# Optimization experiments

Hardware: AMD Instinct MI355X
Metric: run time of the kernel (lower is better)

## Reference

```python
import jax, jax.numpy as jnp
import numpy as np

EMBED = 1024
HEAD = 64
CTX = 2048


def setup_inputs() -> dict:
    key = jax.random.key(0)
    ks = jax.random.split(key, 7)
    scale = 1.0 / np.sqrt(EMBED)
    return {
        "x": jax.random.normal(ks[0], (8, CTX, EMBED), dtype=jnp.float32),
        "Wq": jax.random.normal(ks[1], (EMBED, HEAD), dtype=jnp.float32) * scale,
        "bq": jax.random.normal(ks[2], (HEAD,), dtype=jnp.float32) * 0.01,
        "Wk": jax.random.normal(ks[3], (EMBED, HEAD), dtype=jnp.float32) * scale,
        "bk": jax.random.normal(ks[4], (HEAD,), dtype=jnp.float32) * 0.01,
        "Wv": jax.random.normal(ks[5], (EMBED, HEAD), dtype=jnp.float32) * scale,
        "bv": jax.random.normal(ks[6], (HEAD,), dtype=jnp.float32) * 0.01,
    }


def reference(x, Wq, bq, Wk, bk, Wv, bv):
    # x: [B, T, E]
    q = x @ Wq + bq  # [B, T, H]
    k = x @ Wk + bk
    v = x @ Wv + bv
    scores = jnp.einsum("bqh,bkh->bqk", q, k) / jnp.sqrt(jnp.float32(HEAD))
    T = x.shape[1]
    causal = jnp.tril(jnp.ones((T, T), dtype=bool))
    scores = jnp.where(causal, scores, -jnp.inf)
    attn = jax.nn.softmax(scores, axis=-1)  # dropout=0.0 -> identity
    out = jnp.einsum("bqk,bkh->bqh", attn, v)
    return out
```

## Files before the change

kernel.cpp:

```cpp
#include <hip/hip_runtime.h>
#include <math.h>
#include <stdint.h>

#define BDIM 8
#define TDIM 2048
#define EDIM 1024
#define HDIM 64
#define NCHUNK 144

typedef short bf16x8 __attribute__((ext_vector_type(8)));
typedef float f32x4 __attribute__((ext_vector_type(4)));

__device__ __forceinline__ unsigned short f2bf(float f) {
    uint32_t u = __builtin_bit_cast(uint32_t, f);
    u += 0x7fffu + ((u >> 16) & 1u);
    return (unsigned short)(u >> 16);
}
__device__ __forceinline__ float bf2f(unsigned short s) {
    uint32_t u = ((uint32_t)s) << 16;
    return __builtin_bit_cast(float, u);
}

__global__ __launch_bounds__(256) void prep_w(
    const float* __restrict__ Wq, const float* __restrict__ Wk,
    const float* __restrict__ Wv,
    unsigned short* __restrict__ WqT, unsigned short* __restrict__ WkT,
    unsigned short* __restrict__ WvT)
{
    int id = blockIdx.x * 256 + threadIdx.x;
    int e = id >> 6, h = id & 63;
    int oi = h * EDIM + e;
    WqT[oi] = f2bf(Wq[id]);
    WkT[oi] = f2bf(Wk[id]);
    WvT[oi] = f2bf(Wv[id]);
}

__global__ __launch_bounds__(256) void proj_kernel(
    const float* __restrict__ x,
    const unsigned short* __restrict__ WqT, const unsigned short* __restrict__ WkT,
    const unsigned short* __restrict__ WvT,
    const float* __restrict__ bq, const float* __restrict__ bk,
    const float* __restrict__ bv,
    unsigned short* __restrict__ Qb, unsigned short* __restrict__ Kb,
    unsigned short* __restrict__ VbT)
{
    __shared__ unsigned short Xs[2][64][72];
    __shared__ unsigned short Wqs[2][64][72];
    __shared__ unsigned short Wks[2][64][72];
    __shared__ unsigned short Wvs[2][64][72];

    const int t = threadIdx.x;
    const int lane = t & 63, w = t >> 6, quad = lane >> 4, ln = lane & 15;
    const int row0 = blockIdx.x * 64;
    const int sr = t >> 2;
    const int sc = (t & 3) << 4;

    f32x4 accq[4], acck[4], accv[4];
#pragma unroll
    for (int j = 0; j < 4; ++j) {
        accq[j] = (f32x4)(0.f); acck[j] = (f32x4)(0.f); accv[j] = (f32x4)(0.f);
    }

    const float* xp0  = &x[(size_t)(row0 + sr) * EDIM + sc];
    const size_t wrow = (size_t)sr * EDIM + sc;

    {
        float4 x0 = *(const float4*)(xp0);
        float4 x1 = *(const float4*)(xp0 + 4);
        float4 x2 = *(const float4*)(xp0 + 8);
        float4 x3 = *(const float4*)(xp0 + 12);
        bf16x8 xb0, xb1;
        xb0[0]=(short)f2bf(x0.x); xb0[1]=(short)f2bf(x0.y); xb0[2]=(short)f2bf(x0.z); xb0[3]=(short)f2bf(x0.w);
        xb0[4]=(short)f2bf(x1.x); xb0[5]=(short)f2bf(x1.y); xb0[6]=(short)f2bf(x1.z); xb0[7]=(short)f2bf(x1.w);
        xb1[0]=(short)f2bf(x2.x); xb1[1]=(short)f2bf(x2.y); xb1[2]=(short)f2bf(x2.z); xb1[3]=(short)f2bf(x2.w);
        xb1[4]=(short)f2bf(x3.x); xb1[5]=(short)f2bf(x3.y); xb1[6]=(short)f2bf(x3.z); xb1[7]=(short)f2bf(x3.w);
        *(bf16x8*)&Xs[0][sr][sc]     = xb0;
        *(bf16x8*)&Xs[0][sr][sc + 8] = xb1;
        *(bf16x8*)&Wqs[0][sr][sc]     = *(const bf16x8*)&WqT[wrow];
        *(bf16x8*)&Wqs[0][sr][sc + 8] = *(const bf16x8*)&WqT[wrow + 8];
        *(bf16x8*)&Wks[0][sr][sc]     = *(const bf16x8*)&WkT[wrow];
        *(bf16x8*)&Wks[0][sr][sc + 8] = *(const bf16x8*)&WkT[wrow + 8];
        *(bf16x8*)&Wvs[0][sr][sc]     = *(const bf16x8*)&WvT[wrow];
        *(bf16x8*)&Wvs[0][sr][sc + 8] = *(const bf16x8*)&WvT[wrow + 8];
    }

    for (int kt = 0; kt < EDIM / 64; ++kt) {
        const int cur = kt & 1, nxt = cur ^ 1;

        float4 x0, x1, x2, x3;
        bf16x8 wq0, wq1, wk0, wk1, wv0, wv1;
        if (kt < 15) {
            const float* xp = xp0 + (kt + 1) * 64;
            x0 = *(const float4*)(xp);
            x1 = *(const float4*)(xp + 4);
            x2 = *(const float4*)(xp + 8);
            x3 = *(const float4*)(xp + 12);
            const size_t wo = wrow + (kt + 1) * 64;
            wq0 = *(const bf16x8*)&WqT[wo];
            wq1 = *(const bf16x8*)&WqT[wo + 8];
            wk0 = *(const bf16x8*)&WkT[wo];
            wk1 = *(const bf16x8*)&WkT[wo + 8];
            wv0 = *(const bf16x8*)&WvT[wo];
            wv1 = *(const bf16x8*)&WvT[wo + 8];
        }

        __syncthreads();

        bf16x8 xa0 = *(const bf16x8*)&Xs[cur][16 * w + ln][8 * quad];
        bf16x8 xa1 = *(const bf16x8*)&Xs[cur][16 * w + ln][32 + 8 * quad];
#pragma unroll
        for (int j = 0; j < 4; ++j) {
            bf16x8 w0, w1;
            w0 = *(const bf16x8*)&Wqs[cur][16 * j + ln][8 * quad];
            w1 = *(const bf16x8*)&Wqs[cur][16 * j + ln][32 + 8 * quad];
            accq[j] = __builtin_amdgcn_mfma_f32_16x16x32_bf16(xa0, w0, accq[j], 0, 0, 0);
            accq[j] = __builtin_amdgcn_mfma_f32_16x16x32_bf16(xa1, w1, accq[j], 0, 0, 0);
            w0 = *(const bf16x8*)&Wks[cur][16 * j + ln][8 * quad];
            w1 = *(const bf16x8*)&Wks[cur][16 * j + ln][32 + 8 * quad];
            acck[j] = __builtin_amdgcn_mfma_f32_16x16x32_bf16(xa0, w0, acck[j], 0, 0, 0);
            acck[j] = __builtin_amdgcn_mfma_f32_16x16x32_bf16(xa1, w1, acck[j], 0, 0, 0);
            w0 = *(const bf16x8*)&Wvs[cur][16 * j + ln][8 * quad];
            w1 = *(const bf16x8*)&Wvs[cur][16 * j + ln][32 + 8 * quad];
            accv[j] = __builtin_amdgcn_mfma_f32_16x16x32_bf16(xa0, w0, accv[j], 0, 0, 0);
            accv[j] = __builtin_amdgcn_mfma_f32_16x16x32_bf16(xa1, w1, accv[j], 0, 0, 0);
        }

        if (kt < 15) {
            bf16x8 xb0, xb1;
            xb0[0]=(short)f2bf(x0.x); xb0[1]=(short)f2bf(x0.y); xb0[2]=(short)f2bf(x0.z); xb0[3]=(short)f2bf(x0.w);
            xb0[4]=(short)f2bf(x1.x); xb0[5]=(short)f2bf(x1.y); xb0[6]=(short)f2bf(x1.z); xb0[7]=(short)f2bf(x1.w);
            xb1[0]=(short)f2bf(x2.x); xb1[1]=(short)f2bf(x2.y); xb1[2]=(short)f2bf(x2.z); xb1[3]=(short)f2bf(x2.w);
            xb1[4]=(short)f2bf(x3.x); xb1[5]=(short)f2bf(x3.y); xb1[6]=(short)f2bf(x3.z); xb1[7]=(short)f2bf(x3.w);
            *(bf16x8*)&Xs[nxt][sr][sc]     = xb0;
            *(bf16x8*)&Xs[nxt][sr][sc + 8] = xb1;
            *(bf16x8*)&Wqs[nxt][sr][sc]     = wq0;
            *(bf16x8*)&Wqs[nxt][sr][sc + 8] = wq1;
            *(bf16x8*)&Wks[nxt][sr][sc]     = wk0;
            *(bf16x8*)&Wks[nxt][sr][sc + 8] = wk1;
            *(bf16x8*)&Wvs[nxt][sr][sc]     = wv0;
            *(bf16x8*)&Wvs[nxt][sr][sc + 8] = wv1;
        }
    }

#pragma unroll
    for (int j = 0; j < 4; ++j) {
        int col = 16 * j + ln;
        float bqv = bq[col], bkv = bk[col], bvv = bv[col];
#pragma unroll
        for (int r = 0; r < 4; ++r) {
            size_t row = (size_t)(row0 + 16 * w + 4 * quad + r);
            Qb[row * HDIM + col] = f2bf(accq[j][r] + bqv);
            Kb[row * HDIM + col] = f2bf(acck[j][r] + bkv);
            int bb = (int)(row >> 11);
            int tr = (int)(row & 2047);
            VbT[((size_t)bb * HDIM + col) * TDIM + tr] = f2bf(accv[j][r] + bvv);
        }
    }
}

__global__ __launch_bounds__(256) void attn_partial(
    const unsigned short* __restrict__ Qb, const unsigned short* __restrict__ Kb,
    const unsigned short* __restrict__ VbT,
    unsigned short* __restrict__ PO, float* __restrict__ Pm, float* __restrict__ Pl)
{
    __shared__ unsigned short Ks[2][64][72];
    __shared__ unsigned short VsT[2][64][72];
    __shared__ unsigned short Ps[64][72];

    const int t = threadIdx.x;
    const int lane = t & 63, w = t >> 6, quad = lane >> 4, ln = lane & 15;
    const int f = blockIdx.x;
    const int b = blockIdx.y;

    int g = 0;
    while (f >= 2 * (g + 1) * (g + 2)) ++g;
    const int r_  = f - 2 * g * (g + 1);
    const int iq  = 4 * g + r_ / (g + 1);
    const int ch  = r_ % (g + 1);

    const int q0 = iq * 64;
    const size_t base = (size_t)b * TDIM * HDIM;
    const int sr = t >> 2;
    const int sc = (t & 3) << 4;

    const size_t qrow = base + (size_t)(q0 + 16 * w + ln) * HDIM;
    bf16x8 qa0 = *(const bf16x8*)&Qb[qrow + 8 * quad];
    bf16x8 qa1 = *(const bf16x8*)&Qb[qrow + 32 + 8 * quad];

    f32x4 od[4];
#pragma unroll
    for (int j = 0; j < 4; ++j) od[j] = (f32x4)(0.f);
    float mrow[4], lrow[4];
#pragma unroll
    for (int r = 0; r < 4; ++r) { mrow[r] = -INFINITY; lrow[r] = 0.f; }

    const float scale = 0.125f;
    const int jt0 = 4 * ch;
    int j1 = jt0 + 3; if (j1 > iq) j1 = iq;

    {
        size_t ko = base + (size_t)(jt0 * 64 + sr) * HDIM + sc;
        *(bf16x8*)&Ks[0][sr][sc]     = *(const bf16x8*)&Kb[ko];
        *(bf16x8*)&Ks[0][sr][sc + 8] = *(const bf16x8*)&Kb[ko + 8];
        const unsigned short* vrow =
            &VbT[((size_t)b * HDIM + sr) * TDIM + jt0 * 64 + sc];
        *(bf16x8*)&VsT[0][sr][sc]     = *(const bf16x8*)vrow;
        *(bf16x8*)&VsT[0][sr][sc + 8] = *(const bf16x8*)(vrow + 8);
    }

    for (int jt = jt0; jt <= j1; ++jt) {
        const int cur = (jt - jt0) & 1, nxt = cur ^ 1;

        bf16x8 kn0, kn1, vn0, vn1;
        if (jt < j1) {
            size_t ko = base + (size_t)((jt + 1) * 64 + sr) * HDIM + sc;
            kn0 = *(const bf16x8*)&Kb[ko];
            kn1 = *(const bf16x8*)&Kb[ko + 8];
            const unsigned short* vrow =
                &VbT[((size_t)b * HDIM + sr) * TDIM + (jt + 1) * 64 + sc];
            vn0 = *(const bf16x8*)vrow;
            vn1 = *(const bf16x8*)(vrow + 8);
        }

        __syncthreads();

        f32x4 s[4];
#pragma unroll
        for (int j = 0; j < 4; ++j) {
            bf16x8 kb0 = *(const bf16x8*)&Ks[cur][16 * j + ln][8 * quad];
            bf16x8 kb1 = *(const bf16x8*)&Ks[cur][16 * j + ln][32 + 8 * quad];
            s[j] = (f32x4)(0.f);
            s[j] = __builtin_amdgcn_mfma_f32_16x16x32_bf16(qa0, kb0, s[j], 0, 0, 0);
            s[j] = __builtin_amdgcn_mfma_f32_16x16x32_bf16(qa1, kb1, s[j], 0, 0, 0);
        }

        if (jt == iq) {
#pragma unroll
            for (int j = 0; j < 4; ++j) {
                int kg = jt * 64 + 16 * j + ln;
#pragma unroll
                for (int r = 0; r < 4; ++r) {
                    int qg = q0 + 16 * w + 4 * quad + r;
                    s[j][r] = (kg <= qg) ? s[j][r] * scale : -INFINITY;
                }
            }
        } else {
#pragma unroll
            for (int j = 0; j < 4; ++j)
#pragma unroll
                for (int r = 0; r < 4; ++r) s[j][r] *= scale;
        }

        float mx[4];
#pragma unroll
        for (int r = 0; r < 4; ++r)
            mx[r] = fmaxf(fmaxf(s[0][r], s[1][r]), fmaxf(s[2][r], s[3][r]));
#pragma unroll
        for (int d = 1; d < 16; d <<= 1)
#pragma unroll
            for (int r = 0; r < 4; ++r)
                mx[r] = fmaxf(mx[r], __shfl_xor(mx[r], d));

        float al[4], rs[4];
#pragma unroll
        for (int r = 0; r < 4; ++r) {
            float mn = fmaxf(mrow[r], mx[r]);
            al[r] = __expf(mrow[r] - mn);
            mrow[r] = mn;
            float p0 = __expf(s[0][r] - mn);
            float p1 = __expf(s[1][r] - mn);
            float p2 = __expf(s[2][r] - mn);
            float p3 = __expf(s[3][r] - mn);
            s[0][r] = p0; s[1][r] = p1; s[2][r] = p2; s[3][r] = p3;
            rs[r] = (p0 + p1) + (p2 + p3);
        }
#pragma unroll
        for (int d = 1; d < 16; d <<= 1)
#pragma unroll
            for (int r = 0; r < 4; ++r)
                rs[r] += __shfl_xor(rs[r], d);
#pragma unroll
        for (int r = 0; r < 4; ++r) lrow[r] = lrow[r] * al[r] + rs[r];

#pragma unroll
        for (int j = 0; j < 4; ++j)
#pragma unroll
            for (int r = 0; r < 4; ++r) {
                od[j][r] *= al[r];
                Ps[16 * w + 4 * quad + r][16 * j + ln] = f2bf(s[j][r]);
            }

        bf16x8 pa0 = *(const bf16x8*)&Ps[16 * w + ln][8 * quad];
        bf16x8 pa1 = *(const bf16x8*)&Ps[16 * w + ln][32 + 8 * quad];
#pragma unroll
        for (int j = 0; j < 4; ++j) {
            bf16x8 vb0 = *(const bf16x8*)&VsT[cur][16 * j + ln][8 * quad];
            bf16x8 vb1 = *(const bf16x8*)&VsT[cur][16 * j + ln][32 + 8 * quad];
            od[j] = __builtin_amdgcn_mfma_f32_16x16x32_bf16(pa0, vb0, od[j], 0, 0, 0);
            od[j] = __builtin_amdgcn_mfma_f32_16x16x32_bf16(pa1, vb1, od[j], 0, 0, 0);
        }

        if (jt < j1) {
            *(bf16x8*)&Ks[nxt][sr][sc]     = kn0;
            *(bf16x8*)&Ks[nxt][sr][sc + 8] = kn1;
            *(bf16x8*)&VsT[nxt][sr][sc]     = vn0;
            *(bf16x8*)&VsT[nxt][sr][sc + 8] = vn1;
        }
    }

    const size_t p = (size_t)b * NCHUNK + f;
#pragma unroll
    for (int j = 0; j < 4; ++j)
#pragma unroll
        for (int r = 0; r < 4; ++r)
            PO[p * 4096 + (size_t)(16 * w + 4 * quad + r) * 64 + 16 * j + ln] =
                f2bf(od[j][r]);
    if (ln == 0) {
#pragma unroll
        for (int r = 0; r < 4; ++r) {
            Pm[p * 64 + 16 * w + 4 * quad + r] = mrow[r];
            Pl[p * 64 + 16 * w + 4 * quad + r] = lrow[r];
        }
    }
}

__global__ __launch_bounds__(256) void attn_combine(
    const unsigned short* __restrict__ PO, const float* __restrict__ Pm,
    const float* __restrict__ Pl, float* __restrict__ out)
{
    const int iq = blockIdx.x, b = blockIdx.y;
    const int g = iq >> 2;
    const int nch = g + 1;
    const int fbase = 2 * g * (g + 1) + (iq - 4 * g) * (g + 1);
    const int t = threadIdx.x;
    const int row = t >> 2;
    const int c0 = (t & 3) << 4;
    const size_t pbase = (size_t)b * NCHUNK + fbase;

    float M = -INFINITY;
    for (int c = 0; c < nch; ++c)
        M = fmaxf(M, Pm[(pbase + c) * 64 + row]);

    float a[16];
#pragma unroll
    for (int i = 0; i < 16; ++i) a[i] = 0.f;
    float L = 0.f;
    for (int c = 0; c < nch; ++c) {
        size_t p = pbase + c;
        float sc = __expf(Pm[p * 64 + row] - M);
        L += sc * Pl[p * 64 + row];
        const unsigned short* po = &PO[p * 4096 + (size_t)row * 64 + c0];
        bf16x8 v0 = *(const bf16x8*)(po);
        bf16x8 v1 = *(const bf16x8*)(po + 8);
#pragma unroll
        for (int i = 0; i < 8; ++i) {
            a[i]     += sc * bf2f((unsigned short)v0[i]);
            a[8 + i] += sc * bf2f((unsigned short)v1[i]);
        }
    }
    float li = 1.f / L;
    float4 o0, o1, o2, o3;
    o0.x=a[0]*li;  o0.y=a[1]*li;  o0.z=a[2]*li;  o0.w=a[3]*li;
    o1.x=a[4]*li;  o1.y=a[5]*li;  o1.z=a[6]*li;  o1.w=a[7]*li;
    o2.x=a[8]*li;  o2.y=a[9]*li;  o2.z=a[10]*li; o2.w=a[11]*li;
    o3.x=a[12]*li; o3.y=a[13]*li; o3.z=a[14]*li; o3.w=a[15]*li;
    float* op = &out[((size_t)b * TDIM + (size_t)iq * 64 + row) * HDIM + c0];
    *(float4*)(op)      = o0;
    *(float4*)(op + 4)  = o1;
    *(float4*)(op + 8)  = o2;
    *(float4*)(op + 12) = o3;
}

extern "C" void kernel_launch(void* const* d_in, const int* in_sizes, int n_in,
                              void* d_out, int out_size, void* d_ws, size_t ws_size,
                              hipStream_t stream) {
    const float* x  = (const float*)d_in[0];
    const float* Wq = (const float*)d_in[1];
    const float* bq = (const float*)d_in[2];
    const float* Wk = (const float*)d_in[3];
    const float* bk = (const float*)d_in[4];
    const float* Wv = (const float*)d_in[5];
    const float* bv = (const float*)d_in[6];
    float* out = (float*)d_out;

    const size_t n = (size_t)BDIM * TDIM * HDIM;
    unsigned short* Qb  = (unsigned short*)d_ws;
    unsigned short* Kb  = Qb + n;
    unsigned short* VbT = Kb + n;
    unsigned short* WqT = VbT + n;
    unsigned short* WkT = WqT + (size_t)EDIM * HDIM;
    unsigned short* WvT = WkT + (size_t)EDIM * HDIM;
    unsigned short* PO  = WvT + (size_t)EDIM * HDIM;
    float* Pm = (float*)(PO + (size_t)BDIM * NCHUNK * 4096);
    float* Pl = Pm + (size_t)BDIM * NCHUNK * 64;

    prep_w<<<dim3(EDIM * HDIM / 256), 256, 0, stream>>>(Wq, Wk, Wv, WqT, WkT, WvT);
    proj_kernel<<<dim3(BDIM * TDIM / 64), 256, 0, stream>>>(
        x, WqT, WkT, WvT, bq, bk, bv, Qb, Kb, VbT);
    attn_partial<<<dim3(NCHUNK, BDIM), 256, 0, stream>>>(Qb, Kb, VbT, PO, Pm, Pl);
    attn_combine<<<dim3(TDIM / 64, BDIM), 256, 0, stream>>>(PO, Pm, Pl, out);
}
```

Before: 150.9 us.

## Use 8-tile KV chunks and transposed QK^T MFMA to cut softmax shuffles

Doubles the KV chunk length per attention partial block from 4 to 8 tiles, reducing the number of partial blocks (NCHUNK 144→80) and the combine work. Swaps the MFMA operands for QK^T so each lane holds one query row, making the row max/sum reductions a pair of cross-quad shuffles instead of 4x4 shuffle loops. P is packed into LDS with v_cvt_pk_bf16, and s_setprio is raised around the MFMA sections. Fewer blocks means less parallelism and a longer serial loop per block, which can hurt load balance.

```diff
diff --git a/kernel.cpp b/kernel.cpp
--- a/kernel.cpp
+++ b/kernel.cpp
@@ -6,10 +6,11 @@
 #define TDIM 2048
 #define EDIM 1024
 #define HDIM 64
-#define NCHUNK 144
+#define NCHUNK 80
 
 typedef short bf16x8 __attribute__((ext_vector_type(8)));
 typedef float f32x4 __attribute__((ext_vector_type(4)));
+typedef uint32_t u32x2 __attribute__((ext_vector_type(2)));
 
 __device__ __forceinline__ unsigned short f2bf(float f) {
     uint32_t u = __builtin_bit_cast(uint32_t, f);
@@ -19,6 +20,11 @@
 __device__ __forceinline__ float bf2f(unsigned short s) {
     uint32_t u = ((uint32_t)s) << 16;
     return __builtin_bit_cast(float, u);
+}
+__device__ __forceinline__ uint32_t cvt_pk_bf16(float lo, float hi) {
+    uint32_t r;
+    asm("v_cvt_pk_bf16_f32 %0, %1, %2" : "=v"(r) : "v"(lo), "v"(hi));
+    return r;
 }
 
 __global__ __launch_bounds__(256) void prep_w(
@@ -173,9 +179,9 @@
     const int b = blockIdx.y;
 
     int g = 0;
-    while (f >= 2 * (g + 1) * (g + 2)) ++g;
-    const int r_  = f - 2 * g * (g + 1);
-    const int iq  = 4 * g + r_ / (g + 1);
+    while (f >= 4 * (g + 1) * (g + 2)) ++g;
+    const int r_  = f - 4 * g * (g + 1);
+    const int iq  = 8 * g + r_ / (g + 1);
     const int ch  = r_ % (g + 1);
 
     const int q0 = iq * 64;
@@ -190,13 +196,11 @@
     f32x4 od[4];
 #pragma unroll
     for (int j = 0; j < 4; ++j) od[j] = (f32x4)(0.f);
-    float mrow[4], lrow[4];
-#pragma unroll
-    for (int r = 0; r < 4; ++r) { mrow[r] = -INFINITY; lrow[r] = 0.f; }
+    float m_run = -INFINITY, l_run = 0.f;
 
     const float scale = 0.125f;
-    const int jt0 = 4 * ch;
-    int j1 = jt0 + 3; if (j1 > iq) j1 = iq;
+    const int jt0 = 8 * ch;
+    int j1 = jt0 + 7; if (j1 > iq) j1 = iq;
 
     {
         size_t ko = base + (size_t)(jt0 * 64 + sr) * HDIM + sc;
@@ -225,22 +229,24 @@
         __syncthreads();
 
         f32x4 s[4];
+        __builtin_amdgcn_s_setprio(1);
 #pragma unroll
         for (int j = 0; j < 4; ++j) {
             bf16x8 kb0 = *(const bf16x8*)&Ks[cur][16 * j + ln][8 * quad];
             bf16x8 kb1 = *(const bf16x8*)&Ks[cur][16 * j + ln][32 + 8 * quad];
             s[j] = (f32x4)(0.f);
-            s[j] = __builtin_amdgcn_mfma_f32_16x16x32_bf16(qa0, kb0, s[j], 0, 0, 0);
-            s[j] = __builtin_amdgcn_mfma_f32_16x16x32_bf16(qa1, kb1, s[j], 0, 0, 0);
-        }
-
+            s[j] = __builtin_amdgcn_mfma_f32_16x16x32_bf16(kb0, qa0, s[j], 0, 0, 0);
+            s[j] = __builtin_amdgcn_mfma_f32_16x16x32_bf16(kb1, qa1, s[j], 0, 0, 0);
+        }
+        __builtin_amdgcn_s_setprio(0);
+
+        const int qg = q0 + 16 * w + ln;
         if (jt == iq) {
 #pragma unroll
             for (int j = 0; j < 4; ++j) {
-                int kg = jt * 64 + 16 * j + ln;
 #pragma unroll
                 for (int r = 0; r < 4; ++r) {
-                    int qg = q0 + 16 * w + 4 * quad + r;
+                    int kg = jt * 64 + 16 * j + 4 * quad + r;
                     s[j][r] = (kg <= qg) ? s[j][r] * scale : -INFINITY;
                 }
             }
@@ -251,47 +257,53 @@
                 for (int r = 0; r < 4; ++r) s[j][r] *= scale;
         }
 
-        float mx[4];
-#pragma unroll
-        for (int r = 0; r < 4; ++r)
-            mx[r] = fmaxf(fmaxf(s[0][r], s[1][r]), fmaxf(s[2][r], s[3][r]));
-#pragma unroll
-        for (int d = 1; d < 16; d <<= 1)
-#pragma unroll
-            for (int r = 0; r < 4; ++r)
-                mx[r] = fmaxf(mx[r], __shfl_xor(mx[r], d));
-
-        float al[4], rs[4];
+        float mx;
+        {
+            float a0 = fmaxf(fmaxf(s[0][0], s[0][1]), fmaxf(s[0][2], s[0][3]));
+            float a1 = fmaxf(fmaxf(s[1][0], s[1][1]), fmaxf(s[1][2], s[1][3]));
+            float a2 = fmaxf(fmaxf(s[2][0], s[2][1]), fmaxf(s[2][2], s[2][3]));
+            float a3 = fmaxf(fmaxf(s[3][0], s[3][1]), fmaxf(s[3][2], s[3][3]));
+            mx = fmaxf(fmaxf(a0, a1), fmaxf(a2, a3));
+        }
+        mx = fmaxf(mx, __shfl_xor(mx, 16));
+        mx = fmaxf(mx, __shfl_xor(mx, 32));
+
+        float mn = fmaxf(m_run, mx);
+        float al = __expf(m_run - mn);
+        m_run = mn;
+
+        float rs = 0.f;
+#pragma unroll
+        for (int j = 0; j < 4; ++j) {
+            float p0 = __expf(s[j][0] - mn);
+            float p1 = __expf(s[j][1] - mn);
+            float p2 = __expf(s[j][2] - mn);
+            float p3 = __expf(s[j][3] - mn);
+            s[j][0] = p0; s[j][1] = p1; s[j][2] = p2; s[j][3] = p3;
+            rs += (p0 + p1) + (p2 + p3);
+        }
+        rs += __shfl_xor(rs, 16);
+        rs += __shfl_xor(rs, 32);
+        l_run = l_run * al + rs;
+
+#pragma unroll
+        for (int j = 0; j < 4; ++j) {
+            u32x2 pk;
+            pk.x = cvt_pk_bf16(s[j][0], s[j][1]);
+            pk.y = cvt_pk_bf16(s[j][2], s[j][3]);
+            *(u32x2*)&Ps[16 * w + ln][16 * j + 4 * quad] = pk;
+        }
+
 #pragma unroll
         for (int r = 0; r < 4; ++r) {
-            float mn = fmaxf(mrow[r], mx[r]);
-            al[r] = __expf(mrow[r] - mn);
-            mrow[r] = mn;
-            float p0 = __expf(s[0][r] - mn);
-            float p1 = __expf(s[1][r] - mn);
-            float p2 = __expf(s[2][r] - mn);
-            float p3 = __expf(s[3][r] - mn);
-            s[0][r] = p0; s[1][r] = p1; s[2][r] = p2; s[3][r] = p3;
-            rs[r] = (p0 + p1) + (p2 + p3);
-        }
-#pragma unroll
-        for (int d = 1; d < 16; d <<= 1)
-#pragma unroll
-            for (int r = 0; r < 4; ++r)
-                rs[r] += __shfl_xor(rs[r], d);
-#pragma unroll
-        for (int r = 0; r < 4; ++r) lrow[r] = lrow[r] * al[r] + rs[r];
-
-#pragma unroll
-        for (int j = 0; j < 4; ++j)
-#pragma unroll
-            for (int r = 0; r < 4; ++r) {
-                od[j][r] *= al[r];
-                Ps[16 * w + 4 * quad + r][16 * j + ln] = f2bf(s[j][r]);
-            }
+            float alr = __shfl(al, 4 * quad + r);
+#pragma unroll
+            for (int j = 0; j < 4; ++j) od[j][r] *= alr;
+        }
 
         bf16x8 pa0 = *(const bf16x8*)&Ps[16 * w + ln][8 * quad];
         bf16x8 pa1 = *(const bf16x8*)&Ps[16 * w + ln][32 + 8 * quad];
+        __builtin_amdgcn_s_setprio(1);
 #pragma unroll
         for (int j = 0; j < 4; ++j) {
             bf16x8 vb0 = *(const bf16x8*)&VsT[cur][16 * j + ln][8 * quad];
@@ -299,6 +311,7 @@
             od[j] = __builtin_amdgcn_mfma_f32_16x16x32_bf16(pa0, vb0, od[j], 0, 0, 0);
             od[j] = __builtin_amdgcn_mfma_f32_16x16x32_bf16(pa1, vb1, od[j], 0, 0, 0);
         }
+        __builtin_amdgcn_s_setprio(0);
 
         if (jt < j1) {
             *(bf16x8*)&Ks[nxt][sr][sc]     = kn0;
@@ -315,12 +328,9 @@
         for (int r = 0; r < 4; ++r)
             PO[p * 4096 + (size_t)(16 * w + 4 * quad + r) * 64 + 16 * j + ln] =
                 f2bf(od[j][r]);
-    if (ln == 0) {
-#pragma unroll
-        for (int r = 0; r < 4; ++r) {
-            Pm[p * 64 + 16 * w + 4 * quad + r] = mrow[r];
-            Pl[p * 64 + 16 * w + 4 * quad + r] = lrow[r];
-        }
+    if (quad == 0) {
+        Pm[p * 64 + 16 * w + ln] = m_run;
+        Pl[p * 64 + 16 * w + ln] = l_run;
     }
 }
 
@@ -329,9 +339,9 @@
     const float* __restrict__ Pl, float* __restrict__ out)
 {
     const int iq = blockIdx.x, b = blockIdx.y;
-    const int g = iq >> 2;
+    const int g = iq >> 3;
     const int nch = g + 1;
-    const int fbase = 2 * g * (g + 1) + (iq - 4 * g) * (g + 1);
+    const int fbase = 4 * g * (g + 1) + (iq - 8 * g) * (g + 1);
     const int t = threadIdx.x;
     const int row = t >> 2;
     const int c0 = (t & 3) << 4;
```

After: 143.0 us. 1.06x faster.
